# Optimization experiments

Hardware: AMD Instinct MI355X
Metric: run time of the kernel (lower is better)

The kernel has to match this reference:

```python
import jax, jax.numpy as jnp
import numpy as np

N, D, K = 65536, 128, 4096
DECAY = 0.99
COMMIT_W = 1.0
EPS = 1e-5


def setup_inputs() -> dict:
    key = jax.random.key(0)
    k1, k2, k3 = jax.random.split(key, 3)
    x = jax.random.normal(k1, (N, D), dtype=jnp.float32)
    embed = jax.random.normal(k2, (K, D), dtype=jnp.float32)
    cluster_size = jnp.ones((K,), dtype=jnp.float32)
    embed_avg = jax.random.normal(k3, (K, D), dtype=jnp.float32)
    return {"x": x, "embed": embed, "cluster_size": cluster_size, "embed_avg": embed_avg}


def reference(x, embed, cluster_size, embed_avg):
    # --- codebook distance computation + argmin (torch.cdist(...).argmax(-dist)) ---
    x_sq = jnp.sum(x * x, axis=-1, keepdims=True)          # [N, 1]
    e_sq = jnp.sum(embed * embed, axis=-1)                 # [K]
    dist2 = x_sq - 2.0 * jnp.einsum("nd,kd->nk", x, embed) + e_sq  # [N, K]
    embed_ind = jnp.argmin(dist2, axis=-1)                 # [N] int

    # --- gather: quantize ---
    quantize = jnp.take(embed, embed_ind, axis=0)          # [N, D]

    # commitment loss (codes detached) + straight-through estimator
    commit_loss = COMMIT_W * jnp.mean(
        (jax.lax.stop_gradient(quantize) - x) ** 2
    )
    quantize_st = x + jax.lax.stop_gradient(quantize - x)

    # --- EMA codebook update (scatter_add / bincount pattern, no_grad) ---
    xs = jax.lax.stop_gradient(x)
    counts = jax.ops.segment_sum(
        jnp.ones((N,), dtype=jnp.float32), embed_ind, num_segments=K
    )                                                      # bincount [K]
    embed_sum = jax.ops.segment_sum(xs, embed_ind, num_segments=K)  # [K, D]

    new_cluster_size = cluster_size * DECAY + counts * (1.0 - DECAY)
    new_embed_avg = embed_avg * DECAY + embed_sum * (1.0 - DECAY)
    # laplace smoothing of cluster sizes
    n_total = jnp.sum(new_cluster_size)
    smoothed = (new_cluster_size + EPS) / (n_total + K * EPS) * n_total
    new_embed = new_embed_avg / smoothed[:, None]          # [K, D]

    return quantize_st, embed_ind, commit_loss, new_embed, new_cluster_size
```

## Files before the change

kernel.cpp:

```cpp
#include <hip/hip_runtime.h>
#include <math.h>

#define NPTS   65536
#define DIM    128
#define KCODES 4096

constexpr float DECAY_F         = 0.99f;
constexpr float ONE_MINUS_DECAY = 0.01f;
constexpr float EPS_F           = 1e-5f;

constexpr int OFF_IDX  = NPTS * DIM;
constexpr int OFF_LOSS = OFF_IDX + NPTS;
constexpr int OFF_EMB  = OFF_LOSS + 1;
constexpr int OFF_NCS  = OFF_EMB + KCODES * DIM;

typedef _Float16 half8 __attribute__((ext_vector_type(8)));
typedef _Float16 half4 __attribute__((ext_vector_type(4)));
typedef float    f32x4 __attribute__((ext_vector_type(4)));

__global__ __launch_bounds__(256) void vq_prep_kernel(const float* __restrict__ embed,
                                                      float* __restrict__ esq,
                                                      unsigned char* __restrict__ Eimg,
                                                      unsigned long long* __restrict__ rowpack,
                                                      unsigned int* __restrict__ counts,
                                                      float* __restrict__ esum,
                                                      float* __restrict__ out) {
    __shared__ float sq[512];
    int b = blockIdx.x, t = threadIdx.x;

    rowpack[b * 512 + t]       = ~0ULL;
    rowpack[b * 512 + 256 + t] = ~0ULL;
    if (t < 32) counts[b * 32 + t] = 0u;
    if (b == 0 && t == 0) out[OFF_LOSS] = 0.f;

    {
        float4* ez = (float4*)esum;
#pragma unroll
        for (int j = 0; j < 4; ++j) ez[(size_t)b * 1024 + j * 256 + t] = (float4){0.f, 0.f, 0.f, 0.f};
    }

    unsigned char* img = Eimg + ((size_t)b << 14);
#pragma unroll
    for (int it = 0; it < 2; ++it) {
        int idx = t + it * 256;
        int r = idx >> 4, c8 = idx & 15;
        const float4* src = (const float4*)(embed + (size_t)(b * 32 + r) * DIM + c8 * 8);
        float4 v0 = src[0], v1 = src[1];
        float e[8] = {v0.x, v0.y, v0.z, v0.w, v1.x, v1.y, v1.z, v1.w};
        half8 h8, l8;
        float ss = 0.f;
#pragma unroll
        for (int j = 0; j < 8; ++j) {
            _Float16 h = (_Float16)e[j];
            h8[j] = h;
            l8[j] = (_Float16)(e[j] - (float)h);
            ss = fmaf(e[j], e[j], ss);
        }
        int bo = r * 256 + ((c8 * 16) ^ ((r & 7) << 4));
        *(half8*)(img + bo)        = h8;
        *(half8*)(img + 8192 + bo) = l8;
        sq[idx] = ss;
    }
    __syncthreads();
    if (t < 32) {
        float s = 0.f;
#pragma unroll
        for (int c = 0; c < 16; ++c) s += sq[t * 16 + c];
        esq[b * 32 + t] = s;
    }
}

__global__ __launch_bounds__(256, 4)
void vq_main_kernel(const float* __restrict__ x, const float* __restrict__ esq,
                    const unsigned char* __restrict__ Eimg,
                    unsigned long long* __restrict__ rowpack,
                    unsigned int* __restrict__ counts,
                    int* __restrict__ sidx,
                    float* __restrict__ out) {
    __shared__ __align__(16) unsigned char lds[32768];

    const int tid  = threadIdx.x;
    const int l    = tid & 63;
    const int w    = tid >> 6;
    const int mblk = blockIdx.x >> 1;
    const int half = blockIdx.x & 1;
    const int row0 = mblk * 128;

    half8 ahi[2][4], alo[2][4];
#pragma unroll
    for (int ph = 0; ph < 2; ++ph) {
        if (ph) __syncthreads();
        const float4* xg = (const float4*)(x + (size_t)(row0 + ph * 64) * DIM);
#pragma unroll
        for (int it = 0; it < 8; ++it) {
            int i4 = tid + it * 256;
            int r = i4 >> 5, c4 = i4 & 31;
            float4 v = xg[i4];
            float m0 = -2.f * v.x, m1 = -2.f * v.y, m2 = -2.f * v.z, m3 = -2.f * v.w;
            half4 h, lo;
            h[0] = (_Float16)m0; h[1] = (_Float16)m1; h[2] = (_Float16)m2; h[3] = (_Float16)m3;
            lo[0] = (_Float16)(m0 - (float)h[0]); lo[1] = (_Float16)(m1 - (float)h[1]);
            lo[2] = (_Float16)(m2 - (float)h[2]); lo[3] = (_Float16)(m3 - (float)h[3]);
            int bo = r * 256 + ((c4 * 8) ^ ((r & 7) << 4));
            *(half4*)(lds + bo)         = h;
            *(half4*)(lds + 16384 + bo) = lo;
        }
        __syncthreads();
        if ((w >> 1) == ph) {
#pragma unroll
            for (int rf = 0; rf < 2; ++rf)
#pragma unroll
                for (int ks = 0; ks < 4; ++ks) {
                    int rloc = (w & 1) * 32 + rf * 16 + (l & 15);
                    int bo = rloc * 256 + ((ks * 64 + (l >> 4) * 16) ^ ((rloc & 7) << 4));
                    ahi[rf][ks] = *(const half8*)(lds + bo);
                    alo[rf][ks] = *(const half8*)(lds + 16384 + bo);
                }
        }
    }
    __syncthreads();

#define STAGE(P, CT)                                                                     \
    {                                                                                    \
        const unsigned char* gsrc = Eimg + ((size_t)(half * 64 + (CT)) << 14);           \
        _Pragma("unroll")                                                                \
        for (int t = 0; t < 4; ++t) {                                                    \
            __builtin_amdgcn_global_load_lds(                                            \
                (const __attribute__((address_space(1))) unsigned int*)(gsrc + t * 4096 + w * 1024 + l * 16), \
                (__attribute__((address_space(3))) unsigned int*)(lds + (P) * 16384 + t * 4096 + w * 1024),   \
                16, 0, 0);                                                               \
        }                                                                                \
    }

    float minv[2][4];
    int   mini[2][4];
#pragma unroll
    for (int rf = 0; rf < 2; ++rf)
#pragma unroll
        for (int r = 0; r < 4; ++r) { minv[rf][r] = 3.4e38f; mini[rf][r] = 0; }

    STAGE(0, 0);
    __syncthreads();

    for (int ct = 0; ct < 64; ++ct) {
        int p = ct & 1;
        if (ct < 63) STAGE(p ^ 1, ct + 1);
        const unsigned char* bb = lds + p * 16384;

        float ecf[2];
#pragma unroll
        for (int cf = 0; cf < 2; ++cf) ecf[cf] = esq[half * 2048 + ct * 32 + cf * 16 + (l & 15)];

        f32x4 acc[2][2];
#pragma unroll
        for (int rf = 0; rf < 2; ++rf)
#pragma unroll
            for (int cf = 0; cf < 2; ++cf) {
                float e = ecf[cf];
                acc[rf][cf] = (f32x4){e, e, e, e};
            }

        __builtin_amdgcn_s_setprio(1);
#pragma unroll
        for (int ks = 0; ks < 4; ++ks) {
#pragma unroll
            for (int cf = 0; cf < 2; ++cf) {
                int rowb = cf * 16 + (l & 15);
                int bo = rowb * 256 + ((ks * 64 + (l >> 4) * 16) ^ ((rowb & 7) << 4));
                half8 bh = *(const half8*)(bb + bo);
                half8 bl = *(const half8*)(bb + 8192 + bo);
                acc[0][cf] = __builtin_amdgcn_mfma_f32_16x16x32_f16(ahi[0][ks], bh, acc[0][cf], 0, 0, 0);
                acc[1][cf] = __builtin_amdgcn_mfma_f32_16x16x32_f16(ahi[1][ks], bh, acc[1][cf], 0, 0, 0);
                acc[0][cf] = __builtin_amdgcn_mfma_f32_16x16x32_f16(alo[0][ks], bh, acc[0][cf], 0, 0, 0);
                acc[1][cf] = __builtin_amdgcn_mfma_f32_16x16x32_f16(alo[1][ks], bh, acc[1][cf], 0, 0, 0);
                acc[0][cf] = __builtin_amdgcn_mfma_f32_16x16x32_f16(ahi[0][ks], bl, acc[0][cf], 0, 0, 0);
                acc[1][cf] = __builtin_amdgcn_mfma_f32_16x16x32_f16(ahi[1][ks], bl, acc[1][cf], 0, 0, 0);
            }
        }
        __builtin_amdgcn_s_setprio(0);

#pragma unroll
        for (int rf = 0; rf < 2; ++rf)
#pragma unroll
            for (int cf = 0; cf < 2; ++cf) {
                int kidx = half * 2048 + ct * 32 + cf * 16 + (l & 15);
#pragma unroll
                for (int r = 0; r < 4; ++r) {
                    float v = acc[rf][cf][r];
                    if (v < minv[rf][r]) { minv[rf][r] = v; mini[rf][r] = kidx; }
                }
            }

        __syncthreads();
    }

#pragma unroll
    for (int off = 1; off < 16; off <<= 1) {
#pragma unroll
        for (int rf = 0; rf < 2; ++rf)
#pragma unroll
            for (int r = 0; r < 4; ++r) {
                float v2 = __shfl_xor(minv[rf][r], off);
                int   i2 = __shfl_xor(mini[rf][r], off);
                if (v2 < minv[rf][r] || (v2 == minv[rf][r] && i2 < mini[rf][r])) {
                    minv[rf][r] = v2; mini[rf][r] = i2;
                }
            }
    }
    if ((l & 15) == 0) {
#pragma unroll
        for (int rf = 0; rf < 2; ++rf)
#pragma unroll
            for (int r = 0; r < 4; ++r) {
                int row = row0 + w * 32 + rf * 16 + (l >> 4) * 4 + r;
                unsigned int u = __float_as_uint(minv[rf][r]);
                u = (u & 0x80000000u) ? ~u : (u | 0x80000000u);
                unsigned long long key = ((unsigned long long)u << 32) | (unsigned int)mini[rf][r];
                unsigned long long old = atomicMin(&rowpack[row], key);
                if (old != ~0ULL) {
                    unsigned long long fin = old < key ? old : key;
                    int kf = (int)(fin & 0xFFFFFFFFu);
                    out[OFF_IDX + row] = (float)kf;
                    sidx[row] = kf;
                    atomicAdd(&counts[kf], 1u);
                }
            }
    }
}

__global__ __launch_bounds__(256) void vq_scan_kernel(const unsigned int* __restrict__ counts,
                                                      const float* __restrict__ cs,
                                                      float* __restrict__ out,
                                                      int* __restrict__ offsets,
                                                      int* __restrict__ cursor,
                                                      float* __restrict__ inv_sm) {
    __shared__ int   wsum[4];
    __shared__ float wnsum[4];
    int tid = threadIdx.x, l = tid & 63, w = tid >> 6;

    unsigned int c[16];
    float vl[16];
    int   csum = 0;
    float nsum = 0.f;
#pragma unroll
    for (int j = 0; j < 16; ++j) {
        int i = tid * 16 + j;
        c[j] = counts[i];
        csum += (int)c[j];
        float v = fmaf(cs[i], DECAY_F, (float)c[j] * ONE_MINUS_DECAY);
        vl[j] = v;
        nsum += v;
        out[OFF_NCS + i] = v;
    }

    int inc = csum;
#pragma unroll
    for (int off = 1; off < 64; off <<= 1) {
        int t = __shfl_up(inc, off);
        if (l >= off) inc += t;
    }
    float nred = nsum;
#pragma unroll
    for (int off = 32; off >= 1; off >>= 1) nred += __shfl_xor(nred, off);

    if (l == 63) wsum[w] = inc;
    if (l == 0)  wnsum[w] = nred;
    __syncthreads();

    int wpre = 0;
    for (int i = 0; i < w; ++i) wpre += wsum[i];
    float ntot = wnsum[0] + wnsum[1] + wnsum[2] + wnsum[3];
    float num  = ntot + (float)KCODES * EPS_F;

    int off_ = wpre + inc - csum;
#pragma unroll
    for (int j = 0; j < 16; ++j) {
        int i = tid * 16 + j;
        offsets[i] = off_;
        cursor[i]  = off_;
        off_ += (int)c[j];
        inv_sm[i] = num / ((vl[j] + EPS_F) * ntot);
    }
}

__global__ __launch_bounds__(256) void vq_sort_kernel(const int* __restrict__ sidx,
                                                      int* __restrict__ cursor,
                                                      int* __restrict__ rowids,
                                                      int* __restrict__ skey) {
    int r = blockIdx.x * 256 + threadIdx.x;
    int k = sidx[r];
    int pos = atomicAdd(&cursor[k], 1);
    rowids[pos] = r;
    skey[pos]   = k;
}

__global__ __launch_bounds__(256) void vq_segsum_kernel(const float* __restrict__ x,
                                                        const float* __restrict__ embed,
                                                        const int* __restrict__ rowids,
                                                        const int* __restrict__ skey,
                                                        const int* __restrict__ offsets,
                                                        const unsigned int* __restrict__ counts,
                                                        float* __restrict__ esum,
                                                        float* __restrict__ out) {
    __shared__ float buck[64][DIM];
    __shared__ int   rid_s[64], rank_s[64], bcode_s[64];
    __shared__ int   nseg_s;
    __shared__ float lred[4];

    const int tid = threadIdx.x;
    const int w   = tid >> 6, l = tid & 63;
    const int p0  = blockIdx.x * 64;

    {
        float4* bz = (float4*)&buck[0][0];
#pragma unroll
        for (int j = 0; j < 8; ++j) bz[j * 256 + tid] = (float4){0.f, 0.f, 0.f, 0.f};
    }

    if (tid < 64) {
        int p = p0 + tid;
        int k = skey[p];
        rid_s[tid] = rowids[p];
        int f = (tid == 0) ? 1 : (k != skey[p - 1] ? 1 : 0);
        int inc = f;
#pragma unroll
        for (int off = 1; off < 64; off <<= 1) {
            int t = __shfl_up(inc, off);
            if (tid >= off) inc += t;
        }
        int rank = inc - 1;
        rank_s[tid] = rank;
        if (f) bcode_s[rank] = k;
        if (tid == 63) nseg_s = inc;
    }
    __syncthreads();

    float lsum = 0.f;
#pragma unroll 4
    for (int i = 0; i < 16; ++i) {
        int pl = w * 16 + i;
        int r  = rid_s[pl];
        int b  = rank_s[pl];
        int k  = bcode_s[b];
        float2 xv = *(const float2*)(x + (size_t)r * DIM + l * 2);
        float2 ev = *(const float2*)(embed + (size_t)k * DIM + l * 2);
        *(float2*)(out + (size_t)r * DIM + l * 2) = ev;
        atomicAdd(&buck[b][l * 2],     xv.x);
        atomicAdd(&buck[b][l * 2 + 1], xv.y);
        float d0 = ev.x - xv.x, d1 = ev.y - xv.y;
        lsum = fmaf(d0, d0, fmaf(d1, d1, lsum));
    }

#pragma unroll
    for (int s = 32; s >= 1; s >>= 1) lsum += __shfl_xor(lsum, s);
    if (l == 0) lred[w] = lsum;
    __syncthreads();

    int nseg = nseg_s;
    for (int b = w; b < nseg; b += 4) {
        int kb = bcode_s[b];
        int o  = offsets[kb];
        int c  = (int)counts[kb];
        float v0 = buck[b][l * 2], v1 = buck[b][l * 2 + 1];
        if (o >= p0 && o + c <= p0 + 64) {
            *(float2*)(esum + (size_t)kb * DIM + l * 2) = (float2){v0, v1};
        } else {
            atomicAdd(esum + (size_t)kb * DIM + l * 2,     v0);
            atomicAdd(esum + (size_t)kb * DIM + l * 2 + 1, v1);
        }
    }

    if (tid == 0) {
        float bl = (lred[0] + lred[1]) + (lred[2] + lred[3]);
        atomicAdd(out + OFF_LOSS, bl * (1.0f / ((float)NPTS * (float)DIM)));
    }
}

__global__ __launch_bounds__(256) void vq_embed_kernel(const float* __restrict__ eavg,
                                                       const float* __restrict__ esum,
                                                       const float* __restrict__ inv_sm,
                                                       float* __restrict__ out) {
    int i = blockIdx.x * 256 + threadIdx.x;
    int k = i >> 7;
    out[OFF_EMB + i] = fmaf(eavg[i], DECAY_F, esum[i] * ONE_MINUS_DECAY) * inv_sm[k];
}

extern "C" void kernel_launch(void* const* d_in, const int* in_sizes, int n_in,
                              void* d_out, int out_size, void* d_ws, size_t ws_size,
                              hipStream_t stream) {
    const float* x     = (const float*)d_in[0];
    const float* embed = (const float*)d_in[1];
    const float* cs    = (const float*)d_in[2];
    const float* eavg  = (const float*)d_in[3];
    float* out = (float*)d_out;

    unsigned long long* rowpack = (unsigned long long*)d_ws;
    float*         esq     = (float*)(rowpack + NPTS);
    float*         inv_sm  = esq + KCODES;
    unsigned int*  counts  = (unsigned int*)(inv_sm + KCODES);
    int*           offsets = (int*)(counts + KCODES);
    int*           cursor  = offsets + KCODES;
    int*           rowids  = cursor + KCODES;
    int*           sidx    = rowids + NPTS;
    int*           skey    = sidx + NPTS;
    float*         esum    = (float*)(skey + NPTS);
    unsigned char* Eimg    = (unsigned char*)(esum + KCODES * DIM);

    vq_prep_kernel<<<KCODES / 32, 256, 0, stream>>>(embed, esq, Eimg, rowpack, counts, esum, out);
    vq_main_kernel<<<NPTS / 128 * 2, 256, 0, stream>>>(x, esq, Eimg, rowpack, counts, sidx, out);
    vq_scan_kernel<<<1, 256, 0, stream>>>(counts, cs, out, offsets, cursor, inv_sm);
    vq_sort_kernel<<<NPTS / 256, 256, 0, stream>>>(sidx, cursor, rowids, skey);
    vq_segsum_kernel<<<NPTS / 64, 256, 0, stream>>>(x, embed, rowids, skey, offsets, counts, esum, out);
    vq_embed_kernel<<<(KCODES * DIM) / 256, 256, 0, stream>>>(eavg, esum, inv_sm, out);
}
```

Measured before the change: 250.9 us.

## Prefetch esq to LDS, use vmcnt waits for staging, and run-accumulate bucket atomics

```diff
diff --git a/kernel.cpp b/kernel.cpp
--- a/kernel.cpp
+++ b/kernel.cpp
@@ -77,7 +77,7 @@
                     unsigned int* __restrict__ counts,
                     int* __restrict__ sidx,
                     float* __restrict__ out) {
-    __shared__ __align__(16) unsigned char lds[32768];
+    __shared__ __align__(16) unsigned char lds[40960];
 
     const int tid  = threadIdx.x;
     const int l    = tid & 63;
@@ -85,6 +85,13 @@
     const int mblk = blockIdx.x >> 1;
     const int half = blockIdx.x & 1;
     const int row0 = mblk * 128;
+
+    {
+        const float4* eq = (const float4*)(esq + half * 2048);
+        float4* dst = (float4*)(lds + 32768);
+        dst[tid]       = eq[tid];
+        dst[tid + 256] = eq[tid + 256];
+    }
 
     half8 ahi[2][4], alo[2][4];
 #pragma unroll
@@ -139,17 +146,24 @@
 #pragma unroll
         for (int r = 0; r < 4; ++r) { minv[rf][r] = 3.4e38f; mini[rf][r] = 0; }
 
+    const float* esql = (const float*)(lds + 32768);
     STAGE(0, 0);
-    __syncthreads();
 
     for (int ct = 0; ct < 64; ++ct) {
-        int p = ct & 1;
-        if (ct < 63) STAGE(p ^ 1, ct + 1);
+        const int p = ct & 1;
+        if (ct < 63) {
+            STAGE(p ^ 1, ct + 1);
+            asm volatile("s_waitcnt vmcnt(4)" ::: "memory");
+        } else {
+            asm volatile("s_waitcnt vmcnt(0)" ::: "memory");
+        }
+        __builtin_amdgcn_s_barrier();
+
         const unsigned char* bb = lds + p * 16384;
 
         float ecf[2];
-#pragma unroll
-        for (int cf = 0; cf < 2; ++cf) ecf[cf] = esq[half * 2048 + ct * 32 + cf * 16 + (l & 15)];
+        ecf[0] = esql[ct * 32 + (l & 15)];
+        ecf[1] = esql[ct * 32 + 16 + (l & 15)];
 
         f32x4 acc[2][2];
 #pragma unroll
@@ -191,7 +205,7 @@
                 }
             }
 
-        __syncthreads();
+        __builtin_amdgcn_s_barrier();
     }
 
 #pragma unroll
@@ -336,19 +350,30 @@
     __syncthreads();
 
     float lsum = 0.f;
+    {
+        int prevb = rank_s[w * 16];
+        float2 ev = *(const float2*)(embed + (size_t)bcode_s[prevb] * DIM + l * 2);
+        float ra0 = 0.f, ra1 = 0.f;
 #pragma unroll 4
-    for (int i = 0; i < 16; ++i) {
-        int pl = w * 16 + i;
-        int r  = rid_s[pl];
-        int b  = rank_s[pl];
-        int k  = bcode_s[b];
-        float2 xv = *(const float2*)(x + (size_t)r * DIM + l * 2);
-        float2 ev = *(const float2*)(embed + (size_t)k * DIM + l * 2);
-        *(float2*)(out + (size_t)r * DIM + l * 2) = ev;
-        atomicAdd(&buck[b][l * 2],     xv.x);
-        atomicAdd(&buck[b][l * 2 + 1], xv.y);
-        float d0 = ev.x - xv.x, d1 = ev.y - xv.y;
-        lsum = fmaf(d0, d0, fmaf(d1, d1, lsum));
+        for (int i = 0; i < 16; ++i) {
+            int pl = w * 16 + i;
+            int r  = rid_s[pl];
+            int b  = rank_s[pl];
+            if (b != prevb) {
+                atomicAdd(&buck[prevb][l * 2],     ra0);
+                atomicAdd(&buck[prevb][l * 2 + 1], ra1);
+                ra0 = 0.f; ra1 = 0.f;
+                prevb = b;
+                ev = *(const float2*)(embed + (size_t)bcode_s[b] * DIM + l * 2);
+            }
+            float2 xv = *(const float2*)(x + (size_t)r * DIM + l * 2);
+            *(float2*)(out + (size_t)r * DIM + l * 2) = ev;
+            ra0 += xv.x; ra1 += xv.y;
+            float d0 = ev.x - xv.x, d1 = ev.y - xv.y;
+            lsum = fmaf(d0, d0, fmaf(d1, d1, lsum));
+        }
+        atomicAdd(&buck[prevb][l * 2],     ra0);
+        atomicAdd(&buck[prevb][l * 2 + 1], ra1);
     }
 
 #pragma unroll
```

New measurement: 222.2 us. 1.13x faster.
